# Kernel optimization log

Measured on AMD Instinct MI355X. Metric: run time of the kernel, lower is better.

The kernel has to match this reference:

```python
import jax, jax.numpy as jnp
import numpy as np

VOCAB, EMB, HID = 50257, 256, 512
B, S = 64, 512


def setup_inputs() -> dict:
    key = jax.random.key(0)
    ks = jax.random.split(key, 11)
    sc = 0.05
    return {
        "inputs": jax.random.randint(ks[0], (B, S), 0, VOCAB, dtype=jnp.int32),
        "emb": jax.random.normal(ks[1], (VOCAB, EMB), jnp.float32) * sc,
        "Wi": jax.random.normal(ks[2], (EMB, 4 * HID), jnp.float32) * sc,   # kernel, gate order i|f|g|o (Keras)
        "Wh": jax.random.normal(ks[3], (HID, 4 * HID), jnp.float32) * sc,   # recurrent kernel
        "b": jax.random.normal(ks[4], (4 * HID,), jnp.float32) * sc,
        "W1": jax.random.normal(ks[5], (HID, HID), jnp.float32) * sc,
        "b1": jnp.zeros((HID,), jnp.float32),
        "W2": jax.random.normal(ks[6], (HID, HID), jnp.float32) * sc,
        "b2": jnp.zeros((HID,), jnp.float32),
        "W3": jax.random.normal(ks[7], (HID, VOCAB), jnp.float32) * sc,
        "b3": jnp.zeros((VOCAB,), jnp.float32),
    }


def _lstm_final_h(x, Wi, Wh, b):
    # x: [B, S, E] -> final hidden state [B, H]
    Bsz = x.shape[0]
    H = Wh.shape[0]
    h0 = jnp.zeros((Bsz, H), x.dtype)
    c0 = jnp.zeros((Bsz, H), x.dtype)

    def step(carry, xt):
        h, c = carry
        z = xt @ Wi + h @ Wh + b              # [B, 4H]
        i, f, g, o = jnp.split(z, 4, axis=-1)  # Keras gate order: input, forget, cell, output
        i = jax.nn.sigmoid(i)
        f = jax.nn.sigmoid(f)
        g = jnp.tanh(g)
        o = jax.nn.sigmoid(o)
        c = f * c + i * g
        h = o * jnp.tanh(c)
        return (h, c), None

    (h, _), _ = jax.lax.scan(step, (h0, c0), jnp.swapaxes(x, 0, 1))  # scan over time [S, B, E]
    return h


def reference(inputs, emb, Wi, Wh, b, W1, b1, W2, b2, W3, b3):
    src_emb = emb[inputs]                      # [B, S, E] embedding lookup
    enc_hidden = _lstm_final_h(src_emb, Wi, Wh, b)  # [B, H]
    y = jnp.tanh(enc_hidden @ W1 + b1)
    y = jnp.tanh(y @ W2 + b2)
    logits = y @ W3 + b3                       # [B, vocab]
    return jax.nn.log_softmax(logits, axis=-1)
```

## Files before the change

### kernel.cpp

```cpp
#include <hip/hip_runtime.h>
#include <hip/hip_bf16.h>

#define VOCAB 50257
#define EMBD  256
#define HID   512
#define BATCH 64
#define SEQ   512

typedef short bf16x8 __attribute__((ext_vector_type(8)));
typedef float f32x4  __attribute__((ext_vector_type(4)));

__device__ inline short f2b(float f) {
    union { float f; unsigned u; } v; v.f = f;
    unsigned r = v.u + 0x7FFFu + ((v.u >> 16) & 1u);
    return (short)(r >> 16);
}
__device__ inline unsigned pack2_trunc(float lo, float hi) {
    union { float f; unsigned u; } a, b; a.f = lo; b.f = hi;
    return __builtin_amdgcn_perm(b.u, a.u, 0x07060302);
}
__device__ inline float fast_tanh(float x) {
    x = fminf(fmaxf(x, -15.f), 15.f);
    float e = __expf(2.f * x);
    return (e - 1.f) / (e + 1.f);
}
__device__ inline float fast_sig(float x) { return 1.f / (1.f + __expf(-x)); }

__device__ inline void load_x_frags(const float* __restrict__ emb, int idxv, int quad, bf16x8* Ax) {
#pragma unroll
    for (int kt = 0; kt < 8; ++kt) {
        const float* p = emb + (size_t)idxv * EMBD + kt * 32 + quad * 8;
        float4 e0 = *(const float4*)(p);
        float4 e1 = *(const float4*)(p + 4);
        union { bf16x8 v; unsigned u[4]; } f;
        f.u[0] = pack2_trunc(e0.x, e0.y);
        f.u[1] = pack2_trunc(e0.z, e0.w);
        f.u[2] = pack2_trunc(e1.x, e1.y);
        f.u[3] = pack2_trunc(e1.z, e1.w);
        Ax[kt] = f.v;
    }
}

__global__ __launch_bounds__(256, 1) void lstm_kernel(
    const int* __restrict__ idx, const float* __restrict__ emb,
    const float* __restrict__ Wi, const float* __restrict__ Wh,
    const float* __restrict__ bvec,
    unsigned long long* __restrict__ hbuf ,
    unsigned short* __restrict__ hfinal )
{
    const int wgid = blockIdx.x;
    const int grp  = wgid >> 5;
    const int j    = wgid & 31;
    const int tid  = threadIdx.x;
    const int lane = tid & 63;
    const int gate = tid >> 6;
    const int quad = lane >> 4;
    const int l16  = lane & 15;
    const int col  = gate * HID + j * 16 + l16;
    const int arow = grp * 16 + l16;

    __shared__ float gbuf[4][16][16];
    __shared__ __align__(16) unsigned short hstage[16][HID + 8];

    bf16x8 Bh[16], Bx[8];
#pragma unroll
    for (int kt = 0; kt < 16; ++kt)
#pragma unroll
        for (int i = 0; i < 8; ++i)
            Bh[kt][i] = f2b(Wh[(size_t)(kt * 32 + quad * 8 + i) * 2048 + col]);
#pragma unroll
    for (int kt = 0; kt < 8; ++kt)
#pragma unroll
        for (int i = 0; i < 8; ++i)
            Bx[kt][i] = f2b(Wi[(size_t)(kt * 32 + quad * 8 + i) * 2048 + col]);
    const float bv = bvec[col];

    bf16x8 Ax[8];
    load_x_frags(emb, idx[arow * SEQ], quad, Ax);

    const int srow = gate * 4 + quad;

    const int rr = tid >> 3, u8 = tid & 7, c2 = u8 * 2;
    float cs0 = 0.f, cs1 = 0.f;

    for (int t = 0; t < SEQ; ++t) {
        const unsigned long long* rbase =
            hbuf + ((size_t)((t & 1) * 4 + grp) * 16 + srow) * 256 + l16;

        unsigned long long v[16];
        if (t > 0) {
#pragma unroll
            for (int i = 0; i < 16; ++i)
                v[i] = __hip_atomic_load(rbase + i * 16,
                                         __ATOMIC_RELAXED, __HIP_MEMORY_SCOPE_AGENT);
        }

        f32x4 a0 = {0.f, 0.f, 0.f, 0.f}, a1 = {0.f, 0.f, 0.f, 0.f};
#pragma unroll
        for (int kt = 0; kt < 8; kt += 2) {
            a0 = __builtin_amdgcn_mfma_f32_16x16x32_bf16(Ax[kt],     Bx[kt],     a0, 0, 0, 0);
            a1 = __builtin_amdgcn_mfma_f32_16x16x32_bf16(Ax[kt + 1], Bx[kt + 1], a1, 0, 0, 0);
        }

        if (t > 0) {
            const unsigned tg = (unsigned)t;
            while (true) {
                bool ok = true;
#pragma unroll
                for (int i = 0; i < 16; ++i)
                    ok = ok && ((unsigned)(v[i] >> 32) == tg);
                if (__ballot(ok) == ~0ull) break;
#pragma unroll
                for (int i = 0; i < 16; ++i)
                    v[i] = __hip_atomic_load(rbase + i * 16,
                                             __ATOMIC_RELAXED, __HIP_MEMORY_SCOPE_AGENT);
            }
#pragma unroll
            for (int i = 0; i < 16; ++i)
                *(unsigned*)&hstage[srow][(l16 + i * 16) * 2] = (unsigned)v[i];
        }
        __syncthreads();

        if (t > 0) {
#pragma unroll
            for (int kt = 0; kt < 16; kt += 2) {
                bf16x8 ha = *(const bf16x8*)&hstage[l16][kt * 32 + quad * 8];
                bf16x8 hb = *(const bf16x8*)&hstage[l16][(kt + 1) * 32 + quad * 8];
                a0 = __builtin_amdgcn_mfma_f32_16x16x32_bf16(ha, Bh[kt],     a0, 0, 0, 0);
                a1 = __builtin_amdgcn_mfma_f32_16x16x32_bf16(hb, Bh[kt + 1], a1, 0, 0, 0);
            }
        }

#pragma unroll
        for (int r = 0; r < 4; ++r) {
            float z = a0[r] + a1[r] + bv;
            gbuf[gate][quad * 4 + r][l16] = (gate == 2) ? fast_tanh(z) : fast_sig(z);
        }
        __syncthreads();

        if (tid < 128) {
            float h0, h1;
            {
                float i0 = gbuf[0][rr][c2], f0 = gbuf[1][rr][c2];
                float gg = gbuf[2][rr][c2], o0 = gbuf[3][rr][c2];
                float cc = f0 * cs0 + i0 * gg;
                cs0 = cc;
                h0 = o0 * fast_tanh(cc);
            }
            {
                float i1 = gbuf[0][rr][c2 + 1], f1 = gbuf[1][rr][c2 + 1];
                float gg = gbuf[2][rr][c2 + 1], o1 = gbuf[3][rr][c2 + 1];
                float cc = f1 * cs1 + i1 * gg;
                cs1 = cc;
                h1 = o1 * fast_tanh(cc);
            }
            unsigned pv = (unsigned)(unsigned short)f2b(h0) |
                          ((unsigned)(unsigned short)f2b(h1) << 16);
            unsigned long long val = (unsigned long long)pv |
                                     ((unsigned long long)(unsigned)(t + 1) << 32);
            unsigned long long* dst = hbuf +
                ((size_t)(((t + 1) & 1) * 4 + grp) * 16 + rr) * 256 + j * 8 + u8;
            __hip_atomic_store(dst, val, __ATOMIC_RELAXED, __HIP_MEMORY_SCOPE_AGENT);
            if (t == SEQ - 1)
                *(unsigned*)&hfinal[(size_t)(grp * 16 + rr) * HID + j * 16 + c2] = pv;
        }

        if (t + 1 < SEQ) {
            int nx = idx[arow * SEQ + t + 1];
            load_x_frags(emb, nx, quad, Ax);
        }
    }
}

__global__ __launch_bounds__(256, 1) void gemm_tanh_kernel(
    const unsigned short* __restrict__ A, const float* __restrict__ W,
    const float* __restrict__ bias, unsigned short* __restrict__ out)
{
    const int tid = threadIdx.x, lane = tid & 63, wave = tid >> 6;
    const int quad = lane >> 4, l16 = lane & 15;
    const int col = blockIdx.x * 16 + l16;
    bf16x8 Bw[16];
#pragma unroll
    for (int kt = 0; kt < 16; ++kt)
#pragma unroll
        for (int i = 0; i < 8; ++i)
            Bw[kt][i] = f2b(W[(size_t)(kt * 32 + quad * 8 + i) * HID + col]);
    f32x4 acc = {0.f, 0.f, 0.f, 0.f};
#pragma unroll
    for (int kt = 0; kt < 16; ++kt) {
        bf16x8 a = *(const bf16x8*)(A + (size_t)(wave * 16 + l16) * HID + kt * 32 + quad * 8);
        acc = __builtin_amdgcn_mfma_f32_16x16x32_bf16(a, Bw[kt], acc, 0, 0, 0);
    }
    const float bvv = bias[col];
#pragma unroll
    for (int r = 0; r < 4; ++r) {
        float y = fast_tanh(acc[r] + bvv);
        out[(size_t)(wave * 16 + quad * 4 + r) * HID + col] = (unsigned short)f2b(y);
    }
}

__global__ __launch_bounds__(256, 2) void logits_kernel(
    const unsigned short* __restrict__ A, const float* __restrict__ W3,
    const float* __restrict__ b3, float* __restrict__ outL)
{
    const int tid = threadIdx.x, lane = tid & 63, wave = tid >> 6;
    const int quad = lane >> 4, l16 = lane & 15;
    const int c0 = blockIdx.x * 64;
    const int col = c0 + wave * 16 + l16;
    const bool cok = col < VOCAB;
    const int colc = cok ? col : (VOCAB - 1);

    __shared__ unsigned short wt[256][68];

    f32x4 acc[4];
#pragma unroll
    for (int rt = 0; rt < 4; ++rt) acc[rt] = (f32x4){0.f, 0.f, 0.f, 0.f};

    const int kr = tid >> 4;
    const int cg = (tid & 15) * 4;

    for (int kc = 0; kc < 2; ++kc) {
#pragma unroll 4
        for (int it = 0; it < 16; ++it) {
            const int k = it * 16 + kr;
            const int gc = c0 + cg;
            float4 wv;
            if (gc + 3 < VOCAB) {
                wv = *(const float4*)&W3[(size_t)(kc * 256 + k) * VOCAB + gc];
            } else {
                const float* Wr = &W3[(size_t)(kc * 256 + k) * VOCAB];
                wv.x = (gc + 0 < VOCAB) ? Wr[gc + 0] : 0.f;
                wv.y = (gc + 1 < VOCAB) ? Wr[gc + 1] : 0.f;
                wv.z = (gc + 2 < VOCAB) ? Wr[gc + 2] : 0.f;
                wv.w = (gc + 3 < VOCAB) ? Wr[gc + 3] : 0.f;
            }
            unsigned short* d = &wt[k][cg];
            d[0] = (unsigned short)f2b(wv.x);
            d[1] = (unsigned short)f2b(wv.y);
            d[2] = (unsigned short)f2b(wv.z);
            d[3] = (unsigned short)f2b(wv.w);
        }
        __syncthreads();
        bf16x8 Bw[8];
#pragma unroll
        for (int kt = 0; kt < 8; ++kt)
#pragma unroll
            for (int i = 0; i < 8; ++i)
                Bw[kt][i] = (short)wt[kt * 32 + quad * 8 + i][wave * 16 + l16];
#pragma unroll
        for (int rt = 0; rt < 4; ++rt)
#pragma unroll
            for (int kt = 0; kt < 8; ++kt) {
                bf16x8 a = *(const bf16x8*)(A + (size_t)(rt * 16 + l16) * HID +
                                            kc * 256 + kt * 32 + quad * 8);
                acc[rt] = __builtin_amdgcn_mfma_f32_16x16x32_bf16(a, Bw[kt], acc[rt], 0, 0, 0);
            }
        __syncthreads();
    }
    const float bvv = b3[colc];
    if (cok) {
#pragma unroll
        for (int rt = 0; rt < 4; ++rt)
#pragma unroll
            for (int r = 0; r < 4; ++r)
                outL[(size_t)(rt * 16 + quad * 4 + r) * VOCAB + col] = acc[rt][r] + bvv;
    }
}

__global__ __launch_bounds__(256, 1) void lsm_kernel(
    const float* __restrict__ lg, float* __restrict__ out)
{
    const int row = blockIdx.x;
    const float* L = lg + (size_t)row * VOCAB;
    const float4* L4 = (const float4*)L;
    const int nv4 = VOCAB / 4;

    float m = -1e30f;
    for (int i = threadIdx.x; i < nv4; i += 256) {
        float4 v = L4[i];
        m = fmaxf(fmaxf(fmaxf(m, v.x), fmaxf(v.y, v.z)), v.w);
    }
    if (threadIdx.x == 0) m = fmaxf(m, L[VOCAB - 1]);
#pragma unroll
    for (int o = 32; o; o >>= 1) m = fmaxf(m, __shfl_xor(m, o));
    __shared__ float red[4], red2[4];
    if ((threadIdx.x & 63) == 0) red[threadIdx.x >> 6] = m;
    __syncthreads();
    m = fmaxf(fmaxf(red[0], red[1]), fmaxf(red[2], red[3]));

    float s = 0.f;
    for (int i = threadIdx.x; i < nv4; i += 256) {
        float4 v = L4[i];
        s += __expf(v.x - m) + __expf(v.y - m) + __expf(v.z - m) + __expf(v.w - m);
    }
    if (threadIdx.x == 0) s += __expf(L[VOCAB - 1] - m);
#pragma unroll
    for (int o = 32; o; o >>= 1) s += __shfl_xor(s, o);
    if ((threadIdx.x & 63) == 0) red2[threadIdx.x >> 6] = s;
    __syncthreads();
    s = red2[0] + red2[1] + red2[2] + red2[3];
    const float ls = m + __logf(s);

    float* O = out + (size_t)row * VOCAB;
    float4* O4 = (float4*)O;
    for (int i = threadIdx.x; i < nv4; i += 256) {
        float4 v = L4[i];
        O4[i] = (float4){v.x - ls, v.y - ls, v.z - ls, v.w - ls};
    }
    if (threadIdx.x == 0) O[VOCAB - 1] = L[VOCAB - 1] - ls;
}

extern "C" void kernel_launch(void* const* d_in, const int* in_sizes, int n_in,
                              void* d_out, int out_size, void* d_ws, size_t ws_size,
                              hipStream_t stream) {
    (void)in_sizes; (void)n_in; (void)out_size; (void)ws_size;
    const int*   idx = (const int*)d_in[0];
    const float* emb = (const float*)d_in[1];
    const float* Wi  = (const float*)d_in[2];
    const float* Wh  = (const float*)d_in[3];
    const float* b   = (const float*)d_in[4];
    const float* W1  = (const float*)d_in[5];
    const float* b1  = (const float*)d_in[6];
    const float* W2  = (const float*)d_in[7];
    const float* b2  = (const float*)d_in[8];
    const float* W3  = (const float*)d_in[9];
    const float* b3  = (const float*)d_in[10];
    float* out = (float*)d_out;

    char* w = (char*)d_ws;
    unsigned long long* hbuf   = (unsigned long long*)w;
    unsigned short*     y1     = (unsigned short*)w;
    unsigned short*     y2     = (unsigned short*)(w + 65536);
    unsigned short*     hfinal = (unsigned short*)(w + 262144);
    float*              logits = (float*)(w + 262144);

    lstm_kernel<<<128, 256, 0, stream>>>(idx, emb, Wi, Wh, b, hbuf, hfinal);
    gemm_tanh_kernel<<<HID / 16, 256, 0, stream>>>(hfinal, W1, b1, y1);
    gemm_tanh_kernel<<<HID / 16, 256, 0, stream>>>(y1, W2, b2, y2);
    logits_kernel<<<(VOCAB + 63) / 64, 256, 0, stream>>>(y2, W3, b3, logits);
    lsm_kernel<<<BATCH, 256, 0, stream>>>(logits, out);
}
```

Measured before the change: 2.193 ms.

## Interleave gate columns per wave to compute LSTM cell update in registers

Restructures the persistent LSTM kernel so that each 16-column MFMA tile holds the i/f/g/o gates for the same 4 hidden units. The cell update is then done with cross-lane shuffles instead of an LDS gate buffer and a second __syncthreads per step. The grid shrinks to 64 blocks of 512 threads (8 waves), which also changes the cross-block polling pattern. The h staging buffer is double-buffered so that the one remaining barrier per step stays safe. The risk is that the larger blocks and the altered polling layout add latency to the critical recurrent path.

```diff
diff --git a/kernel.cpp b/kernel.cpp
--- a/kernel.cpp
+++ b/kernel.cpp
@@ -41,7 +41,7 @@
     }
 }
 
-__global__ __launch_bounds__(256, 1) void lstm_kernel(
+__global__ __launch_bounds__(512, 2) void lstm_kernel(
     const int* __restrict__ idx, const float* __restrict__ emb,
     const float* __restrict__ Wi, const float* __restrict__ Wh,
     const float* __restrict__ bvec,
@@ -49,49 +49,51 @@
     unsigned short* __restrict__ hfinal )
 {
     const int wgid = blockIdx.x;
-    const int grp  = wgid >> 5;
-    const int j    = wgid & 31;
+    const int grp  = wgid & 3;
+    const int jj   = wgid >> 2;
     const int tid  = threadIdx.x;
     const int lane = tid & 63;
-    const int gate = tid >> 6;
+    const int w    = tid >> 6;
     const int quad = lane >> 4;
     const int l16  = lane & 15;
-    const int col  = gate * HID + j * 16 + l16;
-    const int arow = grp * 16 + l16;
-
-    __shared__ float gbuf[4][16][16];
-    __shared__ __align__(16) unsigned short hstage[16][HID + 8];
+    const int gl   = l16 >> 2;
+    const int cc   = l16 & 3;
+    const int cbase = jj * 32 + w * 4;
+    const int colW  = gl * HID + cbase + cc;
+    const int arow  = grp * 16 + l16;
+
+    __shared__ __align__(16) unsigned short hstage[2][16][520];
 
     bf16x8 Bh[16], Bx[8];
 #pragma unroll
     for (int kt = 0; kt < 16; ++kt)
 #pragma unroll
         for (int i = 0; i < 8; ++i)
-            Bh[kt][i] = f2b(Wh[(size_t)(kt * 32 + quad * 8 + i) * 2048 + col]);
+            Bh[kt][i] = f2b(Wh[(size_t)(kt * 32 + quad * 8 + i) * 2048 + colW]);
 #pragma unroll
     for (int kt = 0; kt < 8; ++kt)
 #pragma unroll
         for (int i = 0; i < 8; ++i)
-            Bx[kt][i] = f2b(Wi[(size_t)(kt * 32 + quad * 8 + i) * 2048 + col]);
-    const float bv = bvec[col];
+            Bx[kt][i] = f2b(Wi[(size_t)(kt * 32 + quad * 8 + i) * 2048 + colW]);
+    const float bv = bvec[colW];
 
     bf16x8 Ax[8];
     load_x_frags(emb, idx[arow * SEQ], quad, Ax);
 
-    const int srow = gate * 4 + quad;
-
-    const int rr = tid >> 3, u8 = tid & 7, c2 = u8 * 2;
-    float cs0 = 0.f, cs1 = 0.f;
+    const int srow  = w * 2 + (lane >> 5);
+    const int sunit = lane & 31;
+
+    float cs[4] = {0.f, 0.f, 0.f, 0.f};
 
     for (int t = 0; t < SEQ; ++t) {
         const unsigned long long* rbase =
-            hbuf + ((size_t)((t & 1) * 4 + grp) * 16 + srow) * 256 + l16;
-
-        unsigned long long v[16];
+            hbuf + ((size_t)((t & 1) * 4 + grp) * 16 + srow) * 256 + sunit;
+
+        unsigned long long v[8];
         if (t > 0) {
 #pragma unroll
-            for (int i = 0; i < 16; ++i)
-                v[i] = __hip_atomic_load(rbase + i * 16,
+            for (int i = 0; i < 8; ++i)
+                v[i] = __hip_atomic_load(rbase + i * 32,
                                          __ATOMIC_RELAXED, __HIP_MEMORY_SCOPE_AGENT);
         }
 
@@ -107,62 +109,67 @@
             while (true) {
                 bool ok = true;
 #pragma unroll
-                for (int i = 0; i < 16; ++i)
+                for (int i = 0; i < 8; ++i)
                     ok = ok && ((unsigned)(v[i] >> 32) == tg);
                 if (__ballot(ok) == ~0ull) break;
 #pragma unroll
-                for (int i = 0; i < 16; ++i)
-                    v[i] = __hip_atomic_load(rbase + i * 16,
+                for (int i = 0; i < 8; ++i)
+                    v[i] = __hip_atomic_load(rbase + i * 32,
                                              __ATOMIC_RELAXED, __HIP_MEMORY_SCOPE_AGENT);
             }
 #pragma unroll
-            for (int i = 0; i < 16; ++i)
-                *(unsigned*)&hstage[srow][(l16 + i * 16) * 2] = (unsigned)v[i];
+            for (int i = 0; i < 8; ++i)
+                *(unsigned*)&hstage[t & 1][srow][(sunit + i * 32) * 2] = (unsigned)v[i];
         }
         __syncthreads();
 
         if (t > 0) {
 #pragma unroll
             for (int kt = 0; kt < 16; kt += 2) {
-                bf16x8 ha = *(const bf16x8*)&hstage[l16][kt * 32 + quad * 8];
-                bf16x8 hb = *(const bf16x8*)&hstage[l16][(kt + 1) * 32 + quad * 8];
+                bf16x8 ha = *(const bf16x8*)&hstage[t & 1][l16][kt * 32 + quad * 8];
+                bf16x8 hb = *(const bf16x8*)&hstage[t & 1][l16][(kt + 1) * 32 + quad * 8];
                 a0 = __builtin_amdgcn_mfma_f32_16x16x32_bf16(ha, Bh[kt],     a0, 0, 0, 0);
                 a1 = __builtin_amdgcn_mfma_f32_16x16x32_bf16(hb, Bh[kt + 1], a1, 0, 0, 0);
             }
         }
 
+        float hreg[4];
 #pragma unroll
         for (int r = 0; r < 4; ++r) {
-            float z = a0[r] + a1[r] + bv;
-            gbuf[gate][quad * 4 + r][l16] = (gate == 2) ? fast_tanh(z) : fast_sig(z);
-        }
-        __syncthreads();
-
-        if (tid < 128) {
-            float h0, h1;
-            {
-                float i0 = gbuf[0][rr][c2], f0 = gbuf[1][rr][c2];
-                float gg = gbuf[2][rr][c2], o0 = gbuf[3][rr][c2];
-                float cc = f0 * cs0 + i0 * gg;
-                cs0 = cc;
-                h0 = o0 * fast_tanh(cc);
-            }
-            {
-                float i1 = gbuf[0][rr][c2 + 1], f1 = gbuf[1][rr][c2 + 1];
-                float gg = gbuf[2][rr][c2 + 1], o1 = gbuf[3][rr][c2 + 1];
-                float cc = f1 * cs1 + i1 * gg;
-                cs1 = cc;
-                h1 = o1 * fast_tanh(cc);
-            }
-            unsigned pv = (unsigned)(unsigned short)f2b(h0) |
-                          ((unsigned)(unsigned short)f2b(h1) << 16);
-            unsigned long long val = (unsigned long long)pv |
-                                     ((unsigned long long)(unsigned)(t + 1) << 32);
+            float z   = a0[r] + a1[r] + bv;
+            float act = (gl == 2) ? fast_tanh(z) : fast_sig(z);
+            float vf  = __shfl_xor(act, 4);
+            float vg  = __shfl_xor(act, 8);
+            float vo  = __shfl_xor(act, 12);
+            float cn  = vf * cs[r] + act * vg;
+            cs[r]     = cn;
+            hreg[r]   = vo * fast_tanh(cn);
+        }
+        unsigned pv[4];
+#pragma unroll
+        for (int r = 0; r < 4; ++r) {
+            float ho = __shfl_xor(hreg[r], 1);
+            pv[r] = (unsigned)(unsigned short)f2b(hreg[r]) |
+                    ((unsigned)(unsigned short)f2b(ho) << 16);
+        }
+
+        if (gl == 0 && (cc & 1) == 0) {
+            const int cp = jj * 16 + w * 2 + (cc >> 1);
             unsigned long long* dst = hbuf +
-                ((size_t)(((t + 1) & 1) * 4 + grp) * 16 + rr) * 256 + j * 8 + u8;
-            __hip_atomic_store(dst, val, __ATOMIC_RELAXED, __HIP_MEMORY_SCOPE_AGENT);
-            if (t == SEQ - 1)
-                *(unsigned*)&hfinal[(size_t)(grp * 16 + rr) * HID + j * 16 + c2] = pv;
+                ((size_t)(((t + 1) & 1) * 4 + grp) * 16 + quad * 4) * 256 + cp;
+#pragma unroll
+            for (int r = 0; r < 4; ++r) {
+                unsigned long long val = (unsigned long long)pv[r] |
+                                         ((unsigned long long)(unsigned)(t + 1) << 32);
+                __hip_atomic_store(dst + (size_t)r * 256, val,
+                                   __ATOMIC_RELAXED, __HIP_MEMORY_SCOPE_AGENT);
+            }
+            if (t == SEQ - 1) {
+#pragma unroll
+                for (int r = 0; r < 4; ++r)
+                    *(unsigned*)&hfinal[(size_t)(grp * 16 + quad * 4 + r) * HID +
+                                        cbase + cc] = pv[r];
+            }
         }
 
         if (t + 1 < SEQ) {
@@ -334,7 +341,7 @@
     unsigned short*     hfinal = (unsigned short*)(w + 262144);
     float*              logits = (float*)(w + 262144);
 
-    lstm_kernel<<<128, 256, 0, stream>>>(idx, emb, Wi, Wh, b, hbuf, hfinal);
+    lstm_kernel<<<64, 512, 0, stream>>>(idx, emb, Wi, Wh, b, hbuf, hfinal);
     gemm_tanh_kernel<<<HID / 16, 256, 0, stream>>>(hfinal, W1, b1, y1);
     gemm_tanh_kernel<<<HID / 16, 256, 0, stream>>>(y1, W2, b2, y2);
     logits_kernel<<<(VOCAB + 63) / 64, 256, 0, stream>>>(y2, W3, b3, logits);
```

Result: slower. 3.362 ms (+53.3%).

## Interleave gate columns per wave so LSTM cell update stays in registers

Applied to the files above, without the earlier changes.

Each wave now owns four hidden columns with all four gates, interleaved in the weight fragments, and the MFMA operands are swapped so every lane's accumulator holds i/f/g/o for one (batch, column) pair. The cell update then runs directly in registers, which removes the gbuf shared-memory round trip and the second __syncthreads per timestep. The h staging buffer is double-buffered by timestep parity so the one remaining barrier is enough. The cost is a shuffle to pair neighbouring columns before the packed store, with only half the lanes storing.

```diff
diff --git a/kernel.cpp b/kernel.cpp
--- a/kernel.cpp
+++ b/kernel.cpp
@@ -50,38 +50,40 @@
 {
     const int wgid = blockIdx.x;
     const int grp  = wgid >> 5;
-    const int j    = wgid & 31;
+    const int jj   = wgid & 31;
     const int tid  = threadIdx.x;
     const int lane = tid & 63;
-    const int gate = tid >> 6;
+    const int w    = tid >> 6;
     const int quad = lane >> 4;
     const int l16  = lane & 15;
-    const int col  = gate * HID + j * 16 + l16;
-    const int arow = grp * 16 + l16;
-
-    __shared__ float gbuf[4][16][16];
-    __shared__ __align__(16) unsigned short hstage[16][HID + 8];
+    const int cbase = jj * 16 + w * 4;
+    const int wcol  = (l16 & 3) * HID + cbase + (l16 >> 2);
+    const int arow  = grp * 16 + l16;
+
+    __shared__ __align__(16) unsigned short hstage[2][16][520];
 
     bf16x8 Bh[16], Bx[8];
 #pragma unroll
     for (int kt = 0; kt < 16; ++kt)
 #pragma unroll
         for (int i = 0; i < 8; ++i)
-            Bh[kt][i] = f2b(Wh[(size_t)(kt * 32 + quad * 8 + i) * 2048 + col]);
+            Bh[kt][i] = f2b(Wh[(size_t)(kt * 32 + quad * 8 + i) * 2048 + wcol]);
 #pragma unroll
     for (int kt = 0; kt < 8; ++kt)
 #pragma unroll
         for (int i = 0; i < 8; ++i)
-            Bx[kt][i] = f2b(Wi[(size_t)(kt * 32 + quad * 8 + i) * 2048 + col]);
-    const float bv = bvec[col];
+            Bx[kt][i] = f2b(Wi[(size_t)(kt * 32 + quad * 8 + i) * 2048 + wcol]);
+
+    float bvr[4];
+#pragma unroll
+    for (int r = 0; r < 4; ++r) bvr[r] = bvec[r * HID + cbase + quad];
 
     bf16x8 Ax[8];
     load_x_frags(emb, idx[arow * SEQ], quad, Ax);
 
-    const int srow = gate * 4 + quad;
-
-    const int rr = tid >> 3, u8 = tid & 7, c2 = u8 * 2;
-    float cs0 = 0.f, cs1 = 0.f;
+    const int srow = w * 4 + quad;
+
+    float cs = 0.f;
 
     for (int t = 0; t < SEQ; ++t) {
         const unsigned long long* rbase =
@@ -98,8 +100,8 @@
         f32x4 a0 = {0.f, 0.f, 0.f, 0.f}, a1 = {0.f, 0.f, 0.f, 0.f};
 #pragma unroll
         for (int kt = 0; kt < 8; kt += 2) {
-            a0 = __builtin_amdgcn_mfma_f32_16x16x32_bf16(Ax[kt],     Bx[kt],     a0, 0, 0, 0);
-            a1 = __builtin_amdgcn_mfma_f32_16x16x32_bf16(Ax[kt + 1], Bx[kt + 1], a1, 0, 0, 0);
+            a0 = __builtin_amdgcn_mfma_f32_16x16x32_bf16(Bx[kt],     Ax[kt],     a0, 0, 0, 0);
+            a1 = __builtin_amdgcn_mfma_f32_16x16x32_bf16(Bx[kt + 1], Ax[kt + 1], a1, 0, 0, 0);
         }
 
         if (t > 0) {
@@ -117,52 +119,39 @@
             }
 #pragma unroll
             for (int i = 0; i < 16; ++i)
-                *(unsigned*)&hstage[srow][(l16 + i * 16) * 2] = (unsigned)v[i];
+                *(unsigned*)&hstage[t & 1][srow][(l16 + i * 16) * 2] = (unsigned)v[i];
         }
         __syncthreads();
 
         if (t > 0) {
 #pragma unroll
             for (int kt = 0; kt < 16; kt += 2) {
-                bf16x8 ha = *(const bf16x8*)&hstage[l16][kt * 32 + quad * 8];
-                bf16x8 hb = *(const bf16x8*)&hstage[l16][(kt + 1) * 32 + quad * 8];
-                a0 = __builtin_amdgcn_mfma_f32_16x16x32_bf16(ha, Bh[kt],     a0, 0, 0, 0);
-                a1 = __builtin_amdgcn_mfma_f32_16x16x32_bf16(hb, Bh[kt + 1], a1, 0, 0, 0);
+                bf16x8 ha = *(const bf16x8*)&hstage[t & 1][l16][kt * 32 + quad * 8];
+                bf16x8 hb = *(const bf16x8*)&hstage[t & 1][l16][(kt + 1) * 32 + quad * 8];
+                a0 = __builtin_amdgcn_mfma_f32_16x16x32_bf16(Bh[kt],     ha, a0, 0, 0, 0);
+                a1 = __builtin_amdgcn_mfma_f32_16x16x32_bf16(Bh[kt + 1], hb, a1, 0, 0, 0);
             }
         }
 
-#pragma unroll
-        for (int r = 0; r < 4; ++r) {
-            float z = a0[r] + a1[r] + bv;
-            gbuf[gate][quad * 4 + r][l16] = (gate == 2) ? fast_tanh(z) : fast_sig(z);
-        }
-        __syncthreads();
-
-        if (tid < 128) {
-            float h0, h1;
-            {
-                float i0 = gbuf[0][rr][c2], f0 = gbuf[1][rr][c2];
-                float gg = gbuf[2][rr][c2], o0 = gbuf[3][rr][c2];
-                float cc = f0 * cs0 + i0 * gg;
-                cs0 = cc;
-                h0 = o0 * fast_tanh(cc);
-            }
-            {
-                float i1 = gbuf[0][rr][c2 + 1], f1 = gbuf[1][rr][c2 + 1];
-                float gg = gbuf[2][rr][c2 + 1], o1 = gbuf[3][rr][c2 + 1];
-                float cc = f1 * cs1 + i1 * gg;
-                cs1 = cc;
-                h1 = o1 * fast_tanh(cc);
-            }
-            unsigned pv = (unsigned)(unsigned short)f2b(h0) |
-                          ((unsigned)(unsigned short)f2b(h1) << 16);
+        float iG = fast_sig (a0[0] + a1[0] + bvr[0]);
+        float fG = fast_sig (a0[1] + a1[1] + bvr[1]);
+        float gG = fast_tanh(a0[2] + a1[2] + bvr[2]);
+        float oG = fast_sig (a0[3] + a1[3] + bvr[3]);
+        cs = fG * cs + iG * gG;
+        float h  = oG * fast_tanh(cs);
+        float hp = __shfl_xor(h, 16);
+        unsigned pv = (unsigned)(unsigned short)f2b(h) |
+                      ((unsigned)(unsigned short)f2b(hp) << 16);
+
+        if ((quad & 1) == 0) {
+            const int cp = jj * 8 + w * 2 + (quad >> 1);
             unsigned long long val = (unsigned long long)pv |
                                      ((unsigned long long)(unsigned)(t + 1) << 32);
             unsigned long long* dst = hbuf +
-                ((size_t)(((t + 1) & 1) * 4 + grp) * 16 + rr) * 256 + j * 8 + u8;
+                ((size_t)(((t + 1) & 1) * 4 + grp) * 16 + l16) * 256 + cp;
             __hip_atomic_store(dst, val, __ATOMIC_RELAXED, __HIP_MEMORY_SCOPE_AGENT);
             if (t == SEQ - 1)
-                *(unsigned*)&hfinal[(size_t)(grp * 16 + rr) * HID + j * 16 + c2] = pv;
+                *(unsigned*)&hfinal[(size_t)(grp * 16 + l16) * HID + cbase + quad] = pv;
         }
 
         if (t + 1 < SEQ) {
```

Result: slower. 2.324 ms (+6.0%).
